# Performance work log

Hardware: AMD Instinct MI355X
Metric: run time of the kernel (lower is better)

Reference implementation:

```python
import jax, jax.numpy as jnp
import numpy as np

D_MODEL = 1024
N_HEADS = 16


def setup_inputs() -> dict:
    key = jax.random.key(0)
    k1, k2, k3 = jax.random.split(key, 3)
    B, S = 2, 2048
    std_qkv = (2.0 / (D_MODEL + 3 * D_MODEL)) ** 0.5
    std_out = (2.0 / (D_MODEL + D_MODEL)) ** 0.5
    X = jax.random.normal(k1, (B, S, D_MODEL), dtype=jnp.float32)
    W_qkv = jax.random.normal(k2, (3 * D_MODEL, D_MODEL), dtype=jnp.float32) * std_qkv
    W_out = jax.random.normal(k3, (D_MODEL, D_MODEL), dtype=jnp.float32) * std_out
    return {"X": X, "W_qkv": W_qkv, "W_out": W_out}


def reference(X, W_qkv, W_out):
    B, S, D = X.shape
    H = N_HEADS
    dk = D // H
    # qkv projection: (..., d) @ W^T -> (..., 3d)
    qkv = jnp.einsum('bsd,ed->bse', X, W_qkv)
    Q, K, V = jnp.split(qkv, 3, axis=-1)
    # split heads: (B, S, H*dk) -> (B, H, S, dk)
    def heads(t):
        return t.reshape(B, S, H, dk).transpose(0, 2, 1, 3)
    Q, K, V = heads(Q), heads(K), heads(V)
    # scaled scores (B, H, S, S)
    scores = jnp.einsum('bhqd,bhkd->bhqk', Q, K) / jnp.sqrt(jnp.float32(dk))
    causal = jnp.tril(jnp.ones((S, S), dtype=bool))
    scores = jnp.where(causal, scores.astype(jnp.float32), -jnp.inf)
    weights = jax.nn.softmax(scores, axis=-1).astype(X.dtype)
    out = jnp.einsum('bhqk,bhkd->bhqd', weights, V)
    out = out.transpose(0, 2, 1, 3).reshape(B, S, D)
    return jnp.einsum('bsd,od->bso', out, W_out)
```

## Files before the change

kernel.cpp:

```cpp
#include <hip/hip_runtime.h>

typedef __bf16 bf16;
typedef __bf16 bf16x4v __attribute__((ext_vector_type(4)));
typedef __bf16 bf16x8 __attribute__((ext_vector_type(8)));
typedef float f32x4 __attribute__((ext_vector_type(4)));

#define MFMA16(a, b, c) __builtin_amdgcn_mfma_f32_16x16x32_bf16((a), (b), (c), 0, 0, 0)

#if __has_builtin(__builtin_amdgcn_exp2f)
#define EXP2(x) __builtin_amdgcn_exp2f(x)
#else
#define EXP2(x) exp2f(x)
#endif

#define SEQ 2048
#define DM 1024
#define NH 16

typedef __attribute__((address_space(3))) unsigned int lds_u32;
typedef __attribute__((address_space(1))) const unsigned int glb_u32;

__device__ __forceinline__ void gld16(const bf16* g, bf16* l) {
    __builtin_amdgcn_global_load_lds((glb_u32*)g, (lds_u32*)l, 16, 0, 0);
}

__global__ __launch_bounds__(256) void cvt_all(const float* __restrict__ X,
                                               const float* __restrict__ Wq,
                                               const float* __restrict__ Wo,
                                               bf16* __restrict__ Xb,
                                               bf16* __restrict__ Wqb,
                                               bf16* __restrict__ Wob) {
    const int i = blockIdx.x * 256 + threadIdx.x;
    const int N1 = (4 * 1024 * 1024) / 4;
    const int N2 = (3 * 1024 * 1024) / 4;
    const float* s; bf16* d; int off;
    if (i < N1)            { s = X;  d = Xb;  off = i; }
    else if (i < N1 + N2)  { s = Wq; d = Wqb; off = i - N1; }
    else                   { s = Wo; d = Wob; off = i - N1 - N2; }
    const float4 v = ((const float4*)s)[off];
    bf16x4v o;
    o.x = (bf16)v.x; o.y = (bf16)v.y; o.z = (bf16)v.z; o.w = (bf16)v.w;
    ((bf16x4v*)d)[off] = o;
}

__global__ __launch_bounds__(256) void gemm_qkv(const bf16* __restrict__ A,
                                                const bf16* __restrict__ B,
                                                bf16* __restrict__ qkbuf,
                                                bf16* __restrict__ vtg) {
    __shared__ bf16 smem[16384];
    bf16* As = smem;
    bf16* Bs = smem + 8192;

    const int K = DM, tid = threadIdx.x;
    const int lane = tid & 63, w = tid >> 6;
    const int quad = lane >> 4, l15 = lane & 15;
    const int wm = (w & 1) * 64, wn = (w >> 1) * 64;

    const int nbx = gridDim.x;
    const int orig = blockIdx.y * nbx + blockIdx.x;
    const int cpx = (nbx * gridDim.y) >> 3;
    const int swz = (orig & 7) * cpx + (orig >> 3);
    const int rowBase = (swz / nbx) * 128, colBase = (swz % nbx) * 128;
    const bool isV = (colBase >= 2 * DM);

    f32x4 acc[4][4] = {};

    auto stage = [&](int k0) {
#pragma unroll
        for (int i = 0; i < 4; ++i) {
            const int c = i * 256 + tid;
            const int row = c >> 3;
            const int sg = (c & 7) ^ (row & 7);
            gld16(A + (size_t)(rowBase + row) * K + k0 + sg * 8,
                  As + (i * 256 + w * 64) * 8);
            gld16(B + (size_t)(colBase + row) * K + k0 + sg * 8,
                  Bs + (i * 256 + w * 64) * 8);
        }
    };

    stage(0);

    for (int k0 = 0; k0 < K; k0 += 64) {
        __syncthreads();

        bf16x8 af[2][4], bfr[2][4];
#pragma unroll
        for (int ks = 0; ks < 2; ++ks)
#pragma unroll
            for (int i = 0; i < 4; ++i) {
                const int ra = wm + i * 16 + l15;
                af[ks][i]  = *(const bf16x8*)(As + ra * 64 + (((ks * 4 + quad) ^ (ra & 7)) * 8));
                const int rb = wn + i * 16 + l15;
                bfr[ks][i] = *(const bf16x8*)(Bs + rb * 64 + (((ks * 4 + quad) ^ (rb & 7)) * 8));
            }

        __syncthreads();

        if (k0 + 64 < K) stage(k0 + 64);

        if (isV) {
#pragma unroll
            for (int ks = 0; ks < 2; ++ks)
#pragma unroll
                for (int i = 0; i < 4; ++i)
#pragma unroll
                    for (int j = 0; j < 4; ++j)
                        acc[i][j] = MFMA16(af[ks][i], bfr[ks][j], acc[i][j]);
        } else {
#pragma unroll
            for (int ks = 0; ks < 2; ++ks)
#pragma unroll
                for (int i = 0; i < 4; ++i)
#pragma unroll
                    for (int j = 0; j < 4; ++j)
                        acc[i][j] = MFMA16(bfr[ks][j], af[ks][i], acc[i][j]);
        }
    }

    if (!isV) {
#pragma unroll
        for (int i = 0; i < 4; ++i)
#pragma unroll
            for (int j = 0; j < 4; ++j) {
                bf16x4v pk;
#pragma unroll
                for (int r = 0; r < 4; ++r) pk[r] = (bf16)acc[i][j][r];
                *(bf16x4v*)(qkbuf + (size_t)(rowBase + wm + i * 16 + l15) * 2048 +
                            colBase + wn + j * 16 + quad * 4) = pk;
            }
    } else {
        bf16* T = smem;
        const int vcolBase = colBase - 2 * DM;
        const int bb = rowBase >> 11;
        const int sBase = rowBase & 2047;
        const int drow0 = tid >> 4, seg = tid & 15;
#pragma unroll
        for (int c = 0; c < 2; ++c) {
            __syncthreads();
            if ((w >> 1) == c) {
#pragma unroll
                for (int i = 0; i < 4; ++i)
#pragma unroll
                    for (int j = 0; j < 4; ++j) {
                        bf16x4v pk;
#pragma unroll
                        for (int r = 0; r < 4; ++r) pk[r] = (bf16)acc[i][j][r];
                        *(bf16x4v*)(T + (j * 16 + l15) * 136 + wm + i * 16 + quad * 4) = pk;
                    }
            }
            __syncthreads();
#pragma unroll
            for (int rr = 0; rr < 4; ++rr) {
                const int drow = rr * 16 + drow0;
                *(bf16x8*)(vtg + (size_t)(bb * DM + vcolBase + c * 64 + drow) * SEQ +
                           sBase + seg * 8) =
                    *(const bf16x8*)(T + drow * 136 + seg * 8);
            }
        }
    }
}

__global__ __launch_bounds__(256) void gemm_out(const bf16* __restrict__ A,
                                                const bf16* __restrict__ B,
                                                float* __restrict__ C) {
    __shared__ bf16 As[64 * 64];
    __shared__ bf16 Bs[128 * 64];

    const int K = DM, N = DM, tid = threadIdx.x;
    const int lane = tid & 63, w = tid >> 6;
    const int quad = lane >> 4, l15 = lane & 15;
    const int wm = (w & 1) * 32, wn = (w >> 1) * 64;

    const int nbx = gridDim.x;
    const int orig = blockIdx.y * nbx + blockIdx.x;
    const int cpx = (nbx * gridDim.y) >> 3;
    const int swz = (orig & 7) * cpx + (orig >> 3);
    const int rowBase = (swz / nbx) * 64, colBase = (swz % nbx) * 128;

    f32x4 acc[2][4] = {};

    auto stage = [&](int k0) {
#pragma unroll
        for (int i = 0; i < 2; ++i) {
            const int c = i * 256 + tid;
            const int row = c >> 3;
            const int sg = (c & 7) ^ (row & 7);
            gld16(A + (size_t)(rowBase + row) * K + k0 + sg * 8,
                  As + (i * 256 + w * 64) * 8);
        }
#pragma unroll
        for (int i = 0; i < 4; ++i) {
            const int c = i * 256 + tid;
            const int row = c >> 3;
            const int sg = (c & 7) ^ (row & 7);
            gld16(B + (size_t)(colBase + row) * K + k0 + sg * 8,
                  Bs + (i * 256 + w * 64) * 8);
        }
    };

    stage(0);

    for (int k0 = 0; k0 < K; k0 += 64) {
        __syncthreads();

        bf16x8 af[2][2], bfr[2][4];
#pragma unroll
        for (int ks = 0; ks < 2; ++ks) {
#pragma unroll
            for (int i = 0; i < 2; ++i) {
                const int ra = wm + i * 16 + l15;
                af[ks][i] = *(const bf16x8*)(As + ra * 64 + (((ks * 4 + quad) ^ (ra & 7)) * 8));
            }
#pragma unroll
            for (int j = 0; j < 4; ++j) {
                const int rb = wn + j * 16 + l15;
                bfr[ks][j] = *(const bf16x8*)(Bs + rb * 64 + (((ks * 4 + quad) ^ (rb & 7)) * 8));
            }
        }

        __syncthreads();

        if (k0 + 64 < K) stage(k0 + 64);

#pragma unroll
        for (int ks = 0; ks < 2; ++ks)
#pragma unroll
            for (int i = 0; i < 2; ++i)
#pragma unroll
                for (int j = 0; j < 4; ++j)
                    acc[i][j] = MFMA16(bfr[ks][j], af[ks][i], acc[i][j]);
    }

#pragma unroll
    for (int i = 0; i < 2; ++i)
#pragma unroll
        for (int j = 0; j < 4; ++j)
            *(f32x4*)(C + (size_t)(rowBase + wm + i * 16 + l15) * N +
                      colBase + wn + j * 16 + quad * 4) = acc[i][j];
}

__global__ __launch_bounds__(256) void attn_fwd(const bf16* __restrict__ qk,
                                                const bf16* __restrict__ vtg,
                                                bf16* __restrict__ ao) {
    __shared__ bf16 Ks[64 * 64];
    __shared__ bf16 Vts[64 * 64];
    __shared__ bf16 Pb[4][16 * 72];

    const int tid = threadIdx.x;
    const int lane = tid & 63, w = tid >> 6;
    const int quad = lane >> 4, l15 = lane & 15;
    const int bh = blockIdx.x;
    const int b = bh >> 4, h = bh & 15;
    const int qb = 31 - blockIdx.y;
    const int g = qb * 64 + w * 16;

    const bf16* qkb   = qk + (size_t)b * SEQ * 2048;
    const bf16* kbase = qkb + DM + h * 64;
    const bf16* vb    = vtg + (size_t)bh * 64 * SEQ;

    auto stage = [&](int k0) {
#pragma unroll
        for (int i = 0; i < 2; ++i) {
            const int c = i * 256 + tid;
            const int row = c >> 3;
            const int sg = (c & 7) ^ (row & 7);
            gld16(kbase + (size_t)(k0 + row) * 2048 + sg * 8,
                  Ks + (i * 256 + w * 64) * 8);
            gld16(vb + (size_t)row * SEQ + k0 + sg * 8,
                  Vts + (i * 256 + w * 64) * 8);
        }
    };

    const int nkt = qb + 1;

    stage(0);

    const float SC = 0.125f * 1.44269504f;
    bf16x8 qlo, qhi;
    {
        const bf16* qp = qkb + (size_t)(g + l15) * 2048 + h * 64 + quad * 8;
        bf16x8 a = *(const bf16x8*)qp, c = *(const bf16x8*)(qp + 32);
#pragma unroll
        for (int i = 0; i < 8; ++i) {
            qlo[i] = (bf16)((float)a[i] * SC);
            qhi[i] = (bf16)((float)c[i] * SC);
        }
    }

    bf16x8 onesf;
#pragma unroll
    for (int i = 0; i < 8; ++i) onesf[i] = (bf16)1.0f;

    f32x4 o[4] = {};
    f32x4 ol = {};

    for (int kt = 0; kt < nkt; ++kt) {
        const int k0 = kt * 64;
        __syncthreads();

        bf16x8 kf[8], vf[8];
#pragma unroll
        for (int t = 0; t < 4; ++t) {
            const int rk = t * 16 + l15;
            kf[2 * t]     = *(const bf16x8*)(Ks + rk * 64 + ((quad ^ (rk & 7)) * 8));
            kf[2 * t + 1] = *(const bf16x8*)(Ks + rk * 64 + (((4 + quad) ^ (rk & 7)) * 8));
            vf[2 * t]     = *(const bf16x8*)(Vts + rk * 64 + ((quad ^ (rk & 7)) * 8));
            vf[2 * t + 1] = *(const bf16x8*)(Vts + rk * 64 + (((4 + quad) ^ (rk & 7)) * 8));
        }

        __syncthreads();

        if (kt + 1 < nkt) stage(k0 + 64);

        f32x4 s[4];
#pragma unroll
        for (int t = 0; t < 4; ++t) {
            f32x4 z = {};
            z = MFMA16(kf[2 * t], qlo, z);
            z = MFMA16(kf[2 * t + 1], qhi, z);
            s[t] = z;
        }

        if (kt == qb) {
#pragma unroll
            for (int t = 0; t < 4; ++t)
#pragma unroll
                for (int r = 0; r < 4; ++r)
                    if (k0 + t * 16 + quad * 4 + r > g + l15) s[t][r] = -1e30f;
        }
        bf16* P = &Pb[w][0];
#pragma unroll
        for (int t = 0; t < 4; ++t) {
            bf16x4v pb4;
#pragma unroll
            for (int r = 0; r < 4; ++r) pb4[r] = (bf16)EXP2(s[t][r]);
            *(bf16x4v*)(P + l15 * 72 + t * 16 + quad * 4) = pb4;
        }

        asm volatile("s_waitcnt lgkmcnt(0)" ::: "memory");

        bf16x8 pa = *(const bf16x8*)(P + l15 * 72 + quad * 8);
        bf16x8 pb = *(const bf16x8*)(P + l15 * 72 + 32 + quad * 8);

#pragma unroll
        for (int dt = 0; dt < 4; ++dt) {
            o[dt] = MFMA16(vf[2 * dt], pa, o[dt]);
            o[dt] = MFMA16(vf[2 * dt + 1], pb, o[dt]);
        }
        ol = MFMA16(onesf, pa, ol);
        ol = MFMA16(onesf, pb, ol);
    }

    const float inv = 1.f / ol[0];
    bf16* a = ao + (size_t)(b * SEQ + g + l15) * DM + h * 64;
#pragma unroll
    for (int dt = 0; dt < 4; ++dt) {
        bf16x4v v;
#pragma unroll
        for (int r = 0; r < 4; ++r) v[r] = (bf16)(o[dt][r] * inv);
        *(bf16x4v*)(a + dt * 16 + quad * 4) = v;
    }
}

extern "C" void kernel_launch(void* const* d_in, const int* in_sizes, int n_in,
                              void* d_out, int out_size, void* d_ws, size_t ws_size,
                              hipStream_t stream) {
    const float* X    = (const float*)d_in[0];
    const float* Wqkv = (const float*)d_in[1];
    const float* Wout = (const float*)d_in[2];
    float* out = (float*)d_out;

    const int M = 2 * SEQ;
    const size_t nX    = (size_t)M * DM;
    const size_t nWqkv = (size_t)3 * DM * DM;
    const size_t nWout = (size_t)DM * DM;
    const size_t nQK   = (size_t)M * 2 * DM;
    const size_t nVT   = (size_t)2 * DM * SEQ;
    const size_t nAO   = (size_t)M * DM;

    if (ws_size < (nX + nWqkv + nWout + nQK + nVT + nAO) * sizeof(bf16)) return;

    bf16* Xb    = (bf16*)d_ws;
    bf16* Wqkvb = Xb + nX;
    bf16* Woutb = Wqkvb + nWqkv;
    bf16* qkbuf = Woutb + nWout;
    bf16* vtg   = qkbuf + nQK;
    bf16* ao    = vtg + nVT;

    const int nCvt4 = (int)((nX + nWqkv + nWout) / 4);
    cvt_all<<<dim3(nCvt4 / 256), 256, 0, stream>>>(X, Wqkv, Wout, Xb, Wqkvb, Woutb);

    gemm_qkv<<<dim3(3 * DM / 128, M / 128), 256, 0, stream>>>(Xb, Wqkvb, qkbuf, vtg);
    attn_fwd<<<dim3(2 * NH, SEQ / 64), 256, 0, stream>>>(qkbuf, vtg, ao);
    gemm_out<<<dim3(DM / 128, M / 64), 256, 0, stream>>>(ao, Woutb, out);
}
```

Baseline: 159.5 us.

## Double block tiles in QKV GEMM and attention to 512 threads for K/V reuse

The QKV GEMM block grows from 128x128 to 256x128 using 8 waves, so each B tile is shared across twice as many rows. The attention kernel now handles 128 query rows per block with 8 waves, so each K/V tile staged into LDS serves twice as many queries. Waves whose rows lie entirely before a key tile skip its compute under a causal liveness check. This halves the number of blocks in both kernels and makes causal work less even across the waves of a block, which can cost occupancy and leave waves idle on diagonal tiles.

```diff
diff --git a/kernel.cpp b/kernel.cpp
--- a/kernel.cpp
+++ b/kernel.cpp
@@ -43,24 +43,24 @@
     ((bf16x4v*)d)[off] = o;
 }
 
-__global__ __launch_bounds__(256) void gemm_qkv(const bf16* __restrict__ A,
-                                                const bf16* __restrict__ B,
-                                                bf16* __restrict__ qkbuf,
-                                                bf16* __restrict__ vtg) {
-    __shared__ bf16 smem[16384];
+__global__ __launch_bounds__(512, 2) void gemm_qkv(const bf16* __restrict__ A,
+                                                   const bf16* __restrict__ B,
+                                                   bf16* __restrict__ qkbuf,
+                                                   bf16* __restrict__ vtg) {
+    __shared__ bf16 smem[24576];
     bf16* As = smem;
-    bf16* Bs = smem + 8192;
+    bf16* Bs = smem + 16384;
 
     const int K = DM, tid = threadIdx.x;
     const int lane = tid & 63, w = tid >> 6;
     const int quad = lane >> 4, l15 = lane & 15;
-    const int wm = (w & 1) * 64, wn = (w >> 1) * 64;
+    const int wm = (w & 3) * 64, wn = (w >> 2) * 64;
 
     const int nbx = gridDim.x;
     const int orig = blockIdx.y * nbx + blockIdx.x;
     const int cpx = (nbx * gridDim.y) >> 3;
     const int swz = (orig & 7) * cpx + (orig >> 3);
-    const int rowBase = (swz / nbx) * 128, colBase = (swz % nbx) * 128;
+    const int rowBase = (swz / nbx) * 256, colBase = (swz % nbx) * 128;
     const bool isV = (colBase >= 2 * DM);
 
     f32x4 acc[4][4] = {};
@@ -68,13 +68,19 @@
     auto stage = [&](int k0) {
 #pragma unroll
         for (int i = 0; i < 4; ++i) {
-            const int c = i * 256 + tid;
+            const int c = i * 512 + tid;
             const int row = c >> 3;
             const int sg = (c & 7) ^ (row & 7);
             gld16(A + (size_t)(rowBase + row) * K + k0 + sg * 8,
-                  As + (i * 256 + w * 64) * 8);
+                  As + (i * 512 + w * 64) * 8);
+        }
+#pragma unroll
+        for (int i = 0; i < 2; ++i) {
+            const int c = i * 512 + tid;
+            const int row = c >> 3;
+            const int sg = (c & 7) ^ (row & 7);
             gld16(B + (size_t)(colBase + row) * K + k0 + sg * 8,
-                  Bs + (i * 256 + w * 64) * 8);
+                  Bs + (i * 512 + w * 64) * 8);
         }
     };
 
@@ -133,11 +139,10 @@
         const int vcolBase = colBase - 2 * DM;
         const int bb = rowBase >> 11;
         const int sBase = rowBase & 2047;
-        const int drow0 = tid >> 4, seg = tid & 15;
 #pragma unroll
         for (int c = 0; c < 2; ++c) {
             __syncthreads();
-            if ((w >> 1) == c) {
+            if ((w >> 2) == c) {
 #pragma unroll
                 for (int i = 0; i < 4; ++i)
 #pragma unroll
@@ -145,16 +150,17 @@
                         bf16x4v pk;
 #pragma unroll
                         for (int r = 0; r < 4; ++r) pk[r] = (bf16)acc[i][j][r];
-                        *(bf16x4v*)(T + (j * 16 + l15) * 136 + wm + i * 16 + quad * 4) = pk;
+                        *(bf16x4v*)(T + (j * 16 + l15) * 264 + wm + i * 16 + quad * 4) = pk;
                     }
             }
             __syncthreads();
 #pragma unroll
-            for (int rr = 0; rr < 4; ++rr) {
-                const int drow = rr * 16 + drow0;
-                *(bf16x8*)(vtg + (size_t)(bb * DM + vcolBase + c * 64 + drow) * SEQ +
-                           sBase + seg * 8) =
-                    *(const bf16x8*)(T + drow * 136 + seg * 8);
+            for (int it = 0; it < 4; ++it) {
+                const int ch = it * 512 + tid;
+                const int d = ch >> 5, sch = ch & 31;
+                *(bf16x8*)(vtg + (size_t)(bb * DM + vcolBase + c * 64 + d) * SEQ +
+                           sBase + sch * 8) =
+                    *(const bf16x8*)(T + d * 264 + sch * 8);
             }
         }
     }
@@ -239,39 +245,33 @@
                       colBase + wn + j * 16 + quad * 4) = acc[i][j];
 }
 
-__global__ __launch_bounds__(256) void attn_fwd(const bf16* __restrict__ qk,
-                                                const bf16* __restrict__ vtg,
-                                                bf16* __restrict__ ao) {
+__global__ __launch_bounds__(512, 4) void attn_fwd(const bf16* __restrict__ qk,
+                                                   const bf16* __restrict__ vtg,
+                                                   bf16* __restrict__ ao) {
     __shared__ bf16 Ks[64 * 64];
     __shared__ bf16 Vts[64 * 64];
-    __shared__ bf16 Pb[4][16 * 72];
+    __shared__ bf16 Pb[8][16 * 72];
 
     const int tid = threadIdx.x;
     const int lane = tid & 63, w = tid >> 6;
     const int quad = lane >> 4, l15 = lane & 15;
     const int bh = blockIdx.x;
     const int b = bh >> 4, h = bh & 15;
-    const int qb = 31 - blockIdx.y;
-    const int g = qb * 64 + w * 16;
+    const int qb = 15 - blockIdx.y;
+    const int g = qb * 128 + w * 16;
 
     const bf16* qkb   = qk + (size_t)b * SEQ * 2048;
     const bf16* kbase = qkb + DM + h * 64;
     const bf16* vb    = vtg + (size_t)bh * 64 * SEQ;
 
     auto stage = [&](int k0) {
-#pragma unroll
-        for (int i = 0; i < 2; ++i) {
-            const int c = i * 256 + tid;
-            const int row = c >> 3;
-            const int sg = (c & 7) ^ (row & 7);
-            gld16(kbase + (size_t)(k0 + row) * 2048 + sg * 8,
-                  Ks + (i * 256 + w * 64) * 8);
-            gld16(vb + (size_t)row * SEQ + k0 + sg * 8,
-                  Vts + (i * 256 + w * 64) * 8);
-        }
+        const int row = tid >> 3;
+        const int sg = (tid & 7) ^ (row & 7);
+        gld16(kbase + (size_t)(k0 + row) * 2048 + sg * 8, Ks + (w * 64) * 8);
+        gld16(vb + (size_t)row * SEQ + k0 + sg * 8,       Vts + (w * 64) * 8);
     };
 
-    const int nkt = qb + 1;
+    const int nkt = 2 * qb + 2;
 
     stage(0);
 
@@ -298,57 +298,63 @@
         const int k0 = kt * 64;
         __syncthreads();
 
+        const bool live = (k0 <= g + 15);
+
         bf16x8 kf[8], vf[8];
-#pragma unroll
-        for (int t = 0; t < 4; ++t) {
-            const int rk = t * 16 + l15;
-            kf[2 * t]     = *(const bf16x8*)(Ks + rk * 64 + ((quad ^ (rk & 7)) * 8));
-            kf[2 * t + 1] = *(const bf16x8*)(Ks + rk * 64 + (((4 + quad) ^ (rk & 7)) * 8));
-            vf[2 * t]     = *(const bf16x8*)(Vts + rk * 64 + ((quad ^ (rk & 7)) * 8));
-            vf[2 * t + 1] = *(const bf16x8*)(Vts + rk * 64 + (((4 + quad) ^ (rk & 7)) * 8));
+        if (live) {
+#pragma unroll
+            for (int t = 0; t < 4; ++t) {
+                const int rk = t * 16 + l15;
+                kf[2 * t]     = *(const bf16x8*)(Ks + rk * 64 + ((quad ^ (rk & 7)) * 8));
+                kf[2 * t + 1] = *(const bf16x8*)(Ks + rk * 64 + (((4 + quad) ^ (rk & 7)) * 8));
+                vf[2 * t]     = *(const bf16x8*)(Vts + rk * 64 + ((quad ^ (rk & 7)) * 8));
+                vf[2 * t + 1] = *(const bf16x8*)(Vts + rk * 64 + (((4 + quad) ^ (rk & 7)) * 8));
+            }
         }
 
         __syncthreads();
 
         if (kt + 1 < nkt) stage(k0 + 64);
 
-        f32x4 s[4];
-#pragma unroll
-        for (int t = 0; t < 4; ++t) {
-            f32x4 z = {};
-            z = MFMA16(kf[2 * t], qlo, z);
-            z = MFMA16(kf[2 * t + 1], qhi, z);
-            s[t] = z;
-        }
-
-        if (kt == qb) {
-#pragma unroll
-            for (int t = 0; t < 4; ++t)
-#pragma unroll
-                for (int r = 0; r < 4; ++r)
-                    if (k0 + t * 16 + quad * 4 + r > g + l15) s[t][r] = -1e30f;
-        }
-        bf16* P = &Pb[w][0];
-#pragma unroll
-        for (int t = 0; t < 4; ++t) {
-            bf16x4v pb4;
-#pragma unroll
-            for (int r = 0; r < 4; ++r) pb4[r] = (bf16)EXP2(s[t][r]);
-            *(bf16x4v*)(P + l15 * 72 + t * 16 + quad * 4) = pb4;
-        }
-
-        asm volatile("s_waitcnt lgkmcnt(0)" ::: "memory");
-
-        bf16x8 pa = *(const bf16x8*)(P + l15 * 72 + quad * 8);
-        bf16x8 pb = *(const bf16x8*)(P + l15 * 72 + 32 + quad * 8);
-
-#pragma unroll
-        for (int dt = 0; dt < 4; ++dt) {
-            o[dt] = MFMA16(vf[2 * dt], pa, o[dt]);
-            o[dt] = MFMA16(vf[2 * dt + 1], pb, o[dt]);
-        }
-        ol = MFMA16(onesf, pa, ol);
-        ol = MFMA16(onesf, pb, ol);
+        if (live) {
+            f32x4 s[4];
+#pragma unroll
+            for (int t = 0; t < 4; ++t) {
+                f32x4 z = {};
+                z = MFMA16(kf[2 * t], qlo, z);
+                z = MFMA16(kf[2 * t + 1], qhi, z);
+                s[t] = z;
+            }
+
+            if (k0 + 63 > g) {
+#pragma unroll
+                for (int t = 0; t < 4; ++t)
+#pragma unroll
+                    for (int r = 0; r < 4; ++r)
+                        if (k0 + t * 16 + quad * 4 + r > g + l15) s[t][r] = -1e30f;
+            }
+            bf16* P = &Pb[w][0];
+#pragma unroll
+            for (int t = 0; t < 4; ++t) {
+                bf16x4v pb4;
+#pragma unroll
+                for (int r = 0; r < 4; ++r) pb4[r] = (bf16)EXP2(s[t][r]);
+                *(bf16x4v*)(P + l15 * 72 + t * 16 + quad * 4) = pb4;
+            }
+
+            asm volatile("s_waitcnt lgkmcnt(0)" ::: "memory");
+
+            bf16x8 pa = *(const bf16x8*)(P + l15 * 72 + quad * 8);
+            bf16x8 pb = *(const bf16x8*)(P + l15 * 72 + 32 + quad * 8);
+
+#pragma unroll
+            for (int dt = 0; dt < 4; ++dt) {
+                o[dt] = MFMA16(vf[2 * dt], pa, o[dt]);
+                o[dt] = MFMA16(vf[2 * dt + 1], pb, o[dt]);
+            }
+            ol = MFMA16(onesf, pa, ol);
+            ol = MFMA16(onesf, pb, ol);
+        }
     }
 
     const float inv = 1.f / ol[0];
@@ -390,7 +396,7 @@
     const int nCvt4 = (int)((nX + nWqkv + nWout) / 4);
     cvt_all<<<dim3(nCvt4 / 256), 256, 0, stream>>>(X, Wqkv, Wout, Xb, Wqkvb, Woutb);
 
-    gemm_qkv<<<dim3(3 * DM / 128, M / 128), 256, 0, stream>>>(Xb, Wqkvb, qkbuf, vtg);
-    attn_fwd<<<dim3(2 * NH, SEQ / 64), 256, 0, stream>>>(qkbuf, vtg, ao);
+    gemm_qkv<<<dim3(3 * DM / 128, M / 256), 512, 0, stream>>>(Xb, Wqkvb, qkbuf, vtg);
+    attn_fwd<<<dim3(2 * NH, SEQ / 128), 512, 0, stream>>>(qkbuf, vtg, ao);
     gemm_out<<<dim3(DM / 128, M / 64), 256, 0, stream>>>(ao, Woutb, out);
 }
```

Measured after the change: 170.0 us. +6.6%, slower.

## Software-pipeline attention PV MFMA one tile behind QK, double-buffer P

Applied to the files above, without the earlier changes.

The P·V product for tile kt-1 is deferred into iteration kt and issued alongside the QK^T MFMAs of tile kt. The P staging buffer is double-buffered per wave, and the V fragments are carried in registers across iterations. This removes the LDS write-then-read stall on P that sat between the exp and the PV MFMAs. It adds s_setprio around the MFMA block and a launch-bounds occupancy hint, at the cost of extra registers (vfp, pa/pb live across the loop), which could spill or reduce occupancy.

```diff
diff --git a/kernel.cpp b/kernel.cpp
--- a/kernel.cpp
+++ b/kernel.cpp
@@ -239,12 +239,12 @@
                       colBase + wn + j * 16 + quad * 4) = acc[i][j];
 }
 
-__global__ __launch_bounds__(256) void attn_fwd(const bf16* __restrict__ qk,
-                                                const bf16* __restrict__ vtg,
-                                                bf16* __restrict__ ao) {
+__global__ __launch_bounds__(256, 4) void attn_fwd(const bf16* __restrict__ qk,
+                                                   const bf16* __restrict__ vtg,
+                                                   bf16* __restrict__ ao) {
     __shared__ bf16 Ks[64 * 64];
     __shared__ bf16 Vts[64 * 64];
-    __shared__ bf16 Pb[4][16 * 72];
+    __shared__ bf16 Pb[4][2][16 * 72];
 
     const int tid = threadIdx.x;
     const int lane = tid & 63, w = tid >> 6;
@@ -293,10 +293,18 @@
 
     f32x4 o[4] = {};
     f32x4 ol = {};
+    bf16x8 vfp[8];
 
     for (int kt = 0; kt < nkt; ++kt) {
         const int k0 = kt * 64;
         __syncthreads();
+
+        bf16x8 pa, pb;
+        if (kt > 0) {
+            const bf16* Pp = &Pb[w][(kt & 1) ^ 1][0];
+            pa = *(const bf16x8*)(Pp + l15 * 72 + quad * 8);
+            pb = *(const bf16x8*)(Pp + l15 * 72 + 32 + quad * 8);
+        }
 
         bf16x8 kf[8], vf[8];
 #pragma unroll
@@ -313,6 +321,7 @@
         if (kt + 1 < nkt) stage(k0 + 64);
 
         f32x4 s[4];
+        __builtin_amdgcn_s_setprio(1);
 #pragma unroll
         for (int t = 0; t < 4; ++t) {
             f32x4 z = {};
@@ -320,6 +329,16 @@
             z = MFMA16(kf[2 * t + 1], qhi, z);
             s[t] = z;
         }
+        if (kt > 0) {
+#pragma unroll
+            for (int dt = 0; dt < 4; ++dt) {
+                o[dt] = MFMA16(vfp[2 * dt], pa, o[dt]);
+                o[dt] = MFMA16(vfp[2 * dt + 1], pb, o[dt]);
+            }
+            ol = MFMA16(onesf, pa, ol);
+            ol = MFMA16(onesf, pb, ol);
+        }
+        __builtin_amdgcn_s_setprio(0);
 
         if (kt == qb) {
 #pragma unroll
@@ -328,7 +347,7 @@
                 for (int r = 0; r < 4; ++r)
                     if (k0 + t * 16 + quad * 4 + r > g + l15) s[t][r] = -1e30f;
         }
-        bf16* P = &Pb[w][0];
+        bf16* P = &Pb[w][kt & 1][0];
 #pragma unroll
         for (int t = 0; t < 4; ++t) {
             bf16x4v pb4;
@@ -337,15 +356,19 @@
             *(bf16x4v*)(P + l15 * 72 + t * 16 + quad * 4) = pb4;
         }
 
-        asm volatile("s_waitcnt lgkmcnt(0)" ::: "memory");
-
-        bf16x8 pa = *(const bf16x8*)(P + l15 * 72 + quad * 8);
-        bf16x8 pb = *(const bf16x8*)(P + l15 * 72 + 32 + quad * 8);
-
+#pragma unroll
+        for (int i = 0; i < 8; ++i) vfp[i] = vf[i];
+    }
+
+    asm volatile("s_waitcnt lgkmcnt(0)" ::: "memory");
+    {
+        const bf16* Pp = &Pb[w][(nkt - 1) & 1][0];
+        bf16x8 pa = *(const bf16x8*)(Pp + l15 * 72 + quad * 8);
+        bf16x8 pb = *(const bf16x8*)(Pp + l15 * 72 + 32 + quad * 8);
 #pragma unroll
         for (int dt = 0; dt < 4; ++dt) {
-            o[dt] = MFMA16(vf[2 * dt], pa, o[dt]);
-            o[dt] = MFMA16(vf[2 * dt + 1], pb, o[dt]);
+            o[dt] = MFMA16(vfp[2 * dt], pa, o[dt]);
+            o[dt] = MFMA16(vfp[2 * dt + 1], pb, o[dt]);
         }
         ol = MFMA16(onesf, pa, ol);
         ol = MFMA16(onesf, pb, ol);
```

New measurement: 266.7 us. 67.2% more time.

## Enlarge QKV GEMM tiles to 256x256 with double-buffered LDS pipeline

Applied to the files above, without the earlier changes.

Rebuilds the QKV projection GEMM around 256x256 output tiles on 512-thread blocks, with each wave computing a 128x64 sub-tile. LDS is double-buffered and the next two K-slices are prefetched with direct global-to-LDS loads, using explicit vmcnt waits and raw barriers so loads overlap MFMA work. The aim is more operand reuse per LDS byte and more latency hiding. In exchange the grid shrinks to 12x16 = 192 blocks, which may under-fill the GPU, and register and LDS pressure (128 KB LDS, 128 accumulator floats per thread) goes up.

```diff
diff --git a/kernel.cpp b/kernel.cpp
--- a/kernel.cpp
+++ b/kernel.cpp
@@ -43,83 +43,103 @@
     ((bf16x4v*)d)[off] = o;
 }
 
-__global__ __launch_bounds__(256) void gemm_qkv(const bf16* __restrict__ A,
+__global__ __launch_bounds__(512) void gemm_qkv(const bf16* __restrict__ A,
                                                 const bf16* __restrict__ B,
                                                 bf16* __restrict__ qkbuf,
                                                 bf16* __restrict__ vtg) {
-    __shared__ bf16 smem[16384];
-    bf16* As = smem;
-    bf16* Bs = smem + 8192;
+    __shared__ bf16 As[2][256 * 64];
+    __shared__ bf16 Bs[2][256 * 64];
 
     const int K = DM, tid = threadIdx.x;
     const int lane = tid & 63, w = tid >> 6;
     const int quad = lane >> 4, l15 = lane & 15;
-    const int wm = (w & 1) * 64, wn = (w >> 1) * 64;
+    const int wr = w >> 2, wc = w & 3;
+    const int wm = wr * 128, wn = wc * 64;
 
     const int nbx = gridDim.x;
     const int orig = blockIdx.y * nbx + blockIdx.x;
     const int cpx = (nbx * gridDim.y) >> 3;
     const int swz = (orig & 7) * cpx + (orig >> 3);
-    const int rowBase = (swz / nbx) * 128, colBase = (swz % nbx) * 128;
+    const int rowBase = (swz / nbx) * 256, colBase = (swz % nbx) * 256;
     const bool isV = (colBase >= 2 * DM);
 
-    f32x4 acc[4][4] = {};
-
-    auto stage = [&](int k0) {
+    f32x4 acc[8][4] = {};
+
+    auto stage = [&](int k0, int buf) {
 #pragma unroll
         for (int i = 0; i < 4; ++i) {
-            const int c = i * 256 + tid;
+            const int c = i * 512 + tid;
             const int row = c >> 3;
             const int sg = (c & 7) ^ (row & 7);
             gld16(A + (size_t)(rowBase + row) * K + k0 + sg * 8,
-                  As + (i * 256 + w * 64) * 8);
+                  &As[buf][0] + (i * 512 + w * 64) * 8);
+        }
+#pragma unroll
+        for (int i = 0; i < 4; ++i) {
+            const int c = i * 512 + tid;
+            const int row = c >> 3;
+            const int sg = (c & 7) ^ (row & 7);
             gld16(B + (size_t)(colBase + row) * K + k0 + sg * 8,
-                  Bs + (i * 256 + w * 64) * 8);
+                  &Bs[buf][0] + (i * 512 + w * 64) * 8);
         }
     };
 
-    stage(0);
-
-    for (int k0 = 0; k0 < K; k0 += 64) {
-        __syncthreads();
-
-        bf16x8 af[2][4], bfr[2][4];
-#pragma unroll
-        for (int ks = 0; ks < 2; ++ks)
-#pragma unroll
-            for (int i = 0; i < 4; ++i) {
+    stage(0, 0);
+    stage(64, 1);
+
+    for (int t = 0; t < 16; ++t) {
+        const int cur = t & 1;
+        if (t < 15) asm volatile("s_waitcnt vmcnt(8)" ::: "memory");
+        else        asm volatile("s_waitcnt vmcnt(0)" ::: "memory");
+        __builtin_amdgcn_s_barrier();
+        __builtin_amdgcn_sched_barrier(0);
+
+        const bf16* Ab = &As[cur][0];
+        const bf16* Bb = &Bs[cur][0];
+
+        bf16x8 bfr[2][4];
+#pragma unroll
+        for (int kk = 0; kk < 2; ++kk)
+#pragma unroll
+            for (int j = 0; j < 4; ++j) {
+                const int rb = wn + j * 16 + l15;
+                bfr[kk][j] = *(const bf16x8*)(Bb + rb * 64 + (((kk * 4 + quad) ^ (rb & 7)) * 8));
+            }
+
+        if (isV) {
+#pragma unroll
+            for (int i = 0; i < 8; ++i) {
                 const int ra = wm + i * 16 + l15;
-                af[ks][i]  = *(const bf16x8*)(As + ra * 64 + (((ks * 4 + quad) ^ (ra & 7)) * 8));
-                const int rb = wn + i * 16 + l15;
-                bfr[ks][i] = *(const bf16x8*)(Bs + rb * 64 + (((ks * 4 + quad) ^ (rb & 7)) * 8));
-            }
-
-        __syncthreads();
-
-        if (k0 + 64 < K) stage(k0 + 64);
-
-        if (isV) {
-#pragma unroll
-            for (int ks = 0; ks < 2; ++ks)
-#pragma unroll
-                for (int i = 0; i < 4; ++i)
-#pragma unroll
-                    for (int j = 0; j < 4; ++j)
-                        acc[i][j] = MFMA16(af[ks][i], bfr[ks][j], acc[i][j]);
+                bf16x8 a0 = *(const bf16x8*)(Ab + ra * 64 + ((quad ^ (ra & 7)) * 8));
+                bf16x8 a1 = *(const bf16x8*)(Ab + ra * 64 + (((4 + quad) ^ (ra & 7)) * 8));
+#pragma unroll
+                for (int j = 0; j < 4; ++j) {
+                    acc[i][j] = MFMA16(a0, bfr[0][j], acc[i][j]);
+                    acc[i][j] = MFMA16(a1, bfr[1][j], acc[i][j]);
+                }
+            }
         } else {
 #pragma unroll
-            for (int ks = 0; ks < 2; ++ks)
-#pragma unroll
-                for (int i = 0; i < 4; ++i)
-#pragma unroll
-                    for (int j = 0; j < 4; ++j)
-                        acc[i][j] = MFMA16(bfr[ks][j], af[ks][i], acc[i][j]);
-        }
+            for (int i = 0; i < 8; ++i) {
+                const int ra = wm + i * 16 + l15;
+                bf16x8 a0 = *(const bf16x8*)(Ab + ra * 64 + ((quad ^ (ra & 7)) * 8));
+                bf16x8 a1 = *(const bf16x8*)(Ab + ra * 64 + (((4 + quad) ^ (ra & 7)) * 8));
+#pragma unroll
+                for (int j = 0; j < 4; ++j) {
+                    acc[i][j] = MFMA16(bfr[0][j], a0, acc[i][j]);
+                    acc[i][j] = MFMA16(bfr[1][j], a1, acc[i][j]);
+                }
+            }
+        }
+
+        __builtin_amdgcn_sched_barrier(0);
+        __builtin_amdgcn_s_barrier();
+        if (t + 2 < 16) stage((t + 2) * 64, cur);
     }
 
     if (!isV) {
 #pragma unroll
-        for (int i = 0; i < 4; ++i)
+        for (int i = 0; i < 8; ++i)
 #pragma unroll
             for (int j = 0; j < 4; ++j) {
                 bf16x4v pk;
@@ -129,32 +149,32 @@
                             colBase + wn + j * 16 + quad * 4) = pk;
             }
     } else {
-        bf16* T = smem;
+        bf16* T = &As[0][0];
         const int vcolBase = colBase - 2 * DM;
         const int bb = rowBase >> 11;
         const int sBase = rowBase & 2047;
-        const int drow0 = tid >> 4, seg = tid & 15;
-#pragma unroll
-        for (int c = 0; c < 2; ++c) {
+#pragma unroll
+        for (int c = 0; c < 4; ++c) {
             __syncthreads();
-            if ((w >> 1) == c) {
-#pragma unroll
-                for (int i = 0; i < 4; ++i)
+            if (wc == c) {
+#pragma unroll
+                for (int i = 0; i < 8; ++i)
 #pragma unroll
                     for (int j = 0; j < 4; ++j) {
                         bf16x4v pk;
 #pragma unroll
                         for (int r = 0; r < 4; ++r) pk[r] = (bf16)acc[i][j][r];
-                        *(bf16x4v*)(T + (j * 16 + l15) * 136 + wm + i * 16 + quad * 4) = pk;
+                        *(bf16x4v*)(T + (j * 16 + l15) * 264 + wm + i * 16 + quad * 4) = pk;
                     }
             }
             __syncthreads();
 #pragma unroll
-            for (int rr = 0; rr < 4; ++rr) {
-                const int drow = rr * 16 + drow0;
-                *(bf16x8*)(vtg + (size_t)(bb * DM + vcolBase + c * 64 + drow) * SEQ +
-                           sBase + seg * 8) =
-                    *(const bf16x8*)(T + drow * 136 + seg * 8);
+            for (int it = 0; it < 4; ++it) {
+                const int ch = it * 512 + tid;
+                const int d = ch >> 5, sch = ch & 31;
+                *(bf16x8*)(vtg + (size_t)(bb * DM + vcolBase + c * 64 + d) * SEQ +
+                           sBase + sch * 8) =
+                    *(const bf16x8*)(T + d * 264 + sch * 8);
             }
         }
     }
@@ -390,7 +410,7 @@
     const int nCvt4 = (int)((nX + nWqkv + nWout) / 4);
     cvt_all<<<dim3(nCvt4 / 256), 256, 0, stream>>>(X, Wqkv, Wout, Xb, Wqkvb, Woutb);
 
-    gemm_qkv<<<dim3(3 * DM / 128, M / 128), 256, 0, stream>>>(Xb, Wqkvb, qkbuf, vtg);
+    gemm_qkv<<<dim3(3 * DM / 256, M / 256), 512, 0, stream>>>(Xb, Wqkvb, qkbuf, vtg);
     attn_fwd<<<dim3(2 * NH, SEQ / 64), 256, 0, stream>>>(qkbuf, vtg, ao);
     gemm_out<<<dim3(DM / 128, M / 64), 256, 0, stream>>>(ao, Woutb, out);
 }
```

Measured after the change: 278.3 us. 1.74x slower.
